# Kernel tuning notes

Hardware: AMD Instinct MI355X
Metric: run time of the kernel (lower is better)

## Reference

```python
import jax, jax.numpy as jnp
import numpy as np

B, T_PAST, FUTURE_N = 128, 1024, 512
IN_F, IP, H, OUT_F = 64, 128, 256, 64


def _init(key, shape, fan_in):
    return (jax.random.uniform(key, shape, jnp.float32) * 2.0 - 1.0) / np.sqrt(fan_in).astype(np.float32)


def setup_inputs() -> dict:
    key = jax.random.key(0)
    ks = jax.random.split(key, 16)
    return {
        "x": jax.random.normal(ks[0], (B, T_PAST, IN_F), jnp.float32),
        "future_n": FUTURE_N,
        # encoder: Linear(IN_F -> IP)
        "enc_W": _init(ks[1], (IP, IN_F), IN_F),
        "enc_b": _init(ks[2], (IP,), IN_F),
        # future encoder: Linear(H -> IP)
        "fut_W": _init(ks[3], (IP, H), H),
        "fut_b": _init(ks[4], (IP,), H),
        # decoder: Linear(H -> OUT_F)
        "dec_W": _init(ks[5], (OUT_F, H), H),
        "dec_b": _init(ks[6], (OUT_F,), H),
        # past LSTMCell(IP, H)
        "pW_ih": _init(ks[7], (4 * H, IP), H),
        "pW_hh": _init(ks[8], (4 * H, H), H),
        "pb_ih": _init(ks[9], (4 * H,), H),
        "pb_hh": _init(ks[10], (4 * H,), H),
        # future LSTMCell(IP, H)
        "fW_ih": _init(ks[11], (4 * H, IP), H),
        "fW_hh": _init(ks[12], (4 * H, H), H),
        "fb_ih": _init(ks[13], (4 * H,), H),
        "fb_hh": _init(ks[14], (4 * H,), H),
    }


def _lstm_cell(xt, h, c, W_ih, W_hh, b_ih, b_hh):
    # torch LSTMCell gate order: i, f, g, o
    gates = xt @ W_ih.T + h @ W_hh.T + (b_ih + b_hh)
    i, f, g, o = jnp.split(gates, 4, axis=-1)
    c_new = jax.nn.sigmoid(f) * c + jax.nn.sigmoid(i) * jnp.tanh(g)
    h_new = jax.nn.sigmoid(o) * jnp.tanh(c_new)
    return h_new, c_new


def reference(x, future_n, enc_W, enc_b, fut_W, fut_b, dec_W, dec_b,
              pW_ih, pW_hh, pb_ih, pb_hh, fW_ih, fW_hh, fb_ih, fb_hh):
    batch = x.shape[0]
    hidden = pW_hh.shape[1]
    h0 = jnp.zeros((batch, hidden), x.dtype)
    c0 = jnp.zeros((batch, hidden), x.dtype)

    encoded = x @ enc_W.T + enc_b  # [B, T, IP]

    def past_step(carry, xt):
        h, c = carry
        h, c = _lstm_cell(xt, h, c, pW_ih, pW_hh, pb_ih, pb_hh)
        return (h, c), h

    (h, c), hs_past = jax.lax.scan(past_step, (h0, c0), jnp.swapaxes(encoded, 0, 1))

    def fut_step(carry, _):
        h, c = carry
        inp = h @ fut_W.T + fut_b
        h, c = _lstm_cell(inp, h, c, fW_ih, fW_hh, fb_ih, fb_hh)
        return (h, c), h

    _, hs_fut = jax.lax.scan(fut_step, (h, c), None, length=future_n)

    hs = jnp.concatenate([hs_past, hs_fut], axis=0)  # [T+F, B, H]
    out = jnp.swapaxes(hs, 0, 1) @ dec_W.T + dec_b  # [B, T+F, OUT_F]
    return out
```

## Files before the change

### kernel.cpp

```cpp
#include <hip/hip_runtime.h>

#define B_    128
#define TPAST 1024
#define FN    512
#define TT    1536
#define INF   64
#define IPF   128
#define HD    256
#define NG    1024
#define OUTF  64

typedef _Float16 f16;
typedef _Float16 f16x8 __attribute__((ext_vector_type(8)));
typedef _Float16 f16x4 __attribute__((ext_vector_type(4)));
typedef float    f32x4 __attribute__((ext_vector_type(4)));

__device__ __forceinline__ float sigm_(float x) {
  return __builtin_amdgcn_rcpf(1.f + __expf(-x));
}
__device__ __forceinline__ float tanh_(float x) {
  return 1.f - 2.f * __builtin_amdgcn_rcpf(1.f + __expf(2.f * x));
}
__device__ __forceinline__ f16x8 oload16(const f16* p) {
  f16x8 v;
  asm volatile("global_load_dwordx4 %0, %1, off\n\ts_waitcnt vmcnt(0)"
               : "=v"(v) : "v"(p));
  return v;
}

extern "C" __global__ void eprep(
    const float* __restrict__ enc_W, const float* __restrict__ enc_b,
    const float* __restrict__ fut_W, const float* __restrict__ fut_b,
    const float* __restrict__ dec_W,
    const float* __restrict__ pW_ih, const float* __restrict__ pW_hh,
    const float* __restrict__ pb_ih, const float* __restrict__ pb_hh,
    const float* __restrict__ fW_ih, const float* __restrict__ fW_hh,
    const float* __restrict__ fb_ih, const float* __restrict__ fb_hh,
    f16* __restrict__ Wp_in, float* __restrict__ bp,
    f16* __restrict__ Wp16, f16* __restrict__ Wf16,
    float* __restrict__ bf, f16* __restrict__ dW16)
{
  int stride = gridDim.x * blockDim.x;
  int gid = blockIdx.x * blockDim.x + threadIdx.x;
  for (int i = gid; i < NG * HD; i += stride) {
    int n = i >> 8, j = i & 255;
    float s = fW_hh[i];
    for (int m = 0; m < IPF; ++m) s += fW_ih[n * IPF + m] * fut_W[m * HD + j];
    Wf16[i] = (f16)s;
    Wp16[i] = (f16)pW_hh[i];
  }
  for (int i = gid; i < NG * INF; i += stride) {
    int n = i >> 6, k = i & 63;
    float s = 0.f;
    for (int m = 0; m < IPF; ++m) s += pW_ih[n * IPF + m] * enc_W[m * INF + k];
    Wp_in[i] = (f16)s;
  }
  for (int i = gid; i < OUTF * HD; i += stride) dW16[i] = (f16)dec_W[i];
  for (int n = gid; n < NG; n += stride) {
    float s1 = pb_ih[n] + pb_hh[n], s2 = fb_ih[n] + fb_hh[n];
    for (int m = 0; m < IPF; ++m) {
      s1 += pW_ih[n * IPF + m] * enc_b[m];
      s2 += fW_ih[n * IPF + m] * fut_b[m];
    }
    bp[n] = s1; bf[n] = s2;
  }
}

extern "C" __global__ __launch_bounds__(64) void epgemm(
    const float* __restrict__ x, const f16* __restrict__ Wp_in,
    const float* __restrict__ bp, f16* __restrict__ P, int t0, int Tc)
{
  int wg = blockIdx.x;
  int tl = wg >> 3, bt = wg & 7;
  int t = t0 + tl;
  int l = (int)threadIdx.x, r = l & 15, g = l >> 4;
  const float* xb = x + ((size_t)(bt * 16 + r) * TPAST + t) * INF;
  f16x8 a[2];
#pragma unroll
  for (int kk = 0; kk < 2; ++kk) {
    const float* px = xb + kk * 32 + g * 8;
    f32x4 v0 = *(const f32x4*)px;
    f32x4 v1 = *(const f32x4*)(px + 4);
#pragma unroll
    for (int e = 0; e < 4; ++e) { a[kk][e] = (f16)v0[e]; a[kk][4 + e] = (f16)v1[e]; }
  }
  for (int nt = 0; nt < 64; ++nt) {
    int n = nt * 16 + r;
    f16x8 b0 = *(const f16x8*)(Wp_in + (size_t)n * INF + g * 8);
    f16x8 b1 = *(const f16x8*)(Wp_in + (size_t)n * INF + 32 + g * 8);
    f32x4 acc = {0.f, 0.f, 0.f, 0.f};
    acc = __builtin_amdgcn_mfma_f32_16x16x32_f16(a[0], b0, acc, 0, 0, 0);
    acc = __builtin_amdgcn_mfma_f32_16x16x32_f16(a[1], b1, acc, 0, 0, 0);
    float bias = bp[n];
    f16x4 hv;
#pragma unroll
    for (int e = 0; e < 4; ++e) hv[e] = (f16)(acc[e] + bias);
    int jh = (n >> 7) & 1;
    int nl = (n >> 8) * 128 + (n & 127);
    f16* Pt = P + (((size_t)(bt * 2 + jh) * Tc + tl) * 512 + nl) * 16;
    *(f16x4*)(Pt + 4 * g) = hv;
  }
}

extern "C" __global__ __launch_bounds__(256, 1)
void erecur(
    const f16* __restrict__ W, const f16* __restrict__ P, int pstep,
    const float* __restrict__ bias,
    f16* __restrict__ hs, f16* __restrict__ h_state, float* __restrict__ c_state,
    f16* __restrict__ Hx, unsigned int* __restrict__ flags,
    int Tc, int seq0, int init_state)
{
  __shared__ f16  Wl[512 * 96];
  __shared__ f16  hb[16 * HD];
  __shared__ float cb[128 * 20];
  __shared__ f16  bl[512];

  int tid = (int)threadIdx.x;
  int w = tid >> 6, l = tid & 63, r = l & 15, g = l >> 4;
  int wg = blockIdx.x;
  int bs = wg >> 1, jh = wg & 1;
  int b0 = bs * 16;

  for (int nl = tid; nl < 512; nl += 256) {
    int n_glob = (nl >> 7) * 256 + jh * 128 + (nl & 127);
#pragma unroll
    for (int c8 = 0; c8 < 12; ++c8) {
      f16x8 v = *(const f16x8*)(W + (size_t)n_glob * HD + 160 + c8 * 8);
      *(f16x8*)&Wl[(nl * 96 + c8 * 8) ^ ((nl & 7) << 3)] = v;
    }
  }
  if (bias) {
    for (int i = tid; i < 512; i += 256) {
      int n_glob = (i >> 7) * 256 + jh * 128 + (i & 127);
      bl[i] = (f16)bias[n_glob];
    }
  }
  f16x8 wf[4][2][5];
#pragma unroll
  for (int ga = 0; ga < 4; ++ga)
#pragma unroll
    for (int s = 0; s < 2; ++s) {
      int n_glob = ga * 256 + jh * 128 + w * 32 + s * 16 + r;
#pragma unroll
      for (int kt = 0; kt < 5; ++kt)
        wf[ga][s][kt] = oload16(W + (size_t)n_glob * HD + kt * 32 + g * 8);
    }
  if (init_state) {
    for (int i = tid; i < 16 * HD; i += 256) hb[i ^ (((i >> 8) & 7) << 3)] = (f16)0.f;
    for (int i = tid; i < 128 * 20; i += 256) cb[i] = 0.f;
  } else {
    for (int i = tid; i < 16 * HD; i += 256) {
      int b = i >> 8, j = i & 255;
      hb[i ^ ((b & 7) << 3)] = h_state[(size_t)(b0 + b) * HD + j];
    }
    for (int i = tid; i < 16 * 128; i += 256) {
      int b = i >> 7, j = i & 127;
      cb[j * 20 + b] = c_state[(size_t)(b0 + b) * HD + jh * 128 + j];
    }
  }
  __syncthreads();

  const f16* Pw = P ? (P + (size_t)wg * Tc * pstep) : nullptr;

  for (int tl = 0; tl < Tc; ++tl) {
    int seq = seq0 + tl;
    f16x4 pv[4][2];
    if (P) {
#pragma unroll
      for (int ga = 0; ga < 4; ++ga)
#pragma unroll
        for (int s = 0; s < 2; ++s) {
          int nl = ga * 128 + w * 32 + s * 16 + r;
          pv[ga][s] = *(const f16x4*)(Pw + nl * 16 + 4 * g);
        }
    }
    f32x4 acc[4][2];
#pragma unroll
    for (int ga = 0; ga < 4; ++ga)
#pragma unroll
      for (int s = 0; s < 2; ++s) acc[ga][s] = f32x4{0.f, 0.f, 0.f, 0.f};

#pragma unroll
    for (int kt = 0; kt < 5; ++kt) {
      f16x8 a = *(const f16x8*)&hb[(r * HD + kt * 32 + g * 8) ^ ((r & 7) << 3)];
#pragma unroll
      for (int ga = 0; ga < 4; ++ga)
#pragma unroll
        for (int s = 0; s < 2; ++s)
          acc[ga][s] = __builtin_amdgcn_mfma_f32_16x16x32_f16(a, wf[ga][s][kt], acc[ga][s], 0, 0, 0);
    }
#pragma unroll
    for (int kt = 5; kt < 8; ++kt) {
      f16x8 a = *(const f16x8*)&hb[(r * HD + kt * 32 + g * 8) ^ ((r & 7) << 3)];
#pragma unroll
      for (int ga = 0; ga < 4; ++ga)
#pragma unroll
        for (int s = 0; s < 2; ++s) {
          int nl = ga * 128 + w * 32 + s * 16 + r;
          f16x8 bw = *(const f16x8*)&Wl[(nl * 96 + (kt - 5) * 32 + g * 8) ^ ((nl & 7) << 3)];
          acc[ga][s] = __builtin_amdgcn_mfma_f32_16x16x32_f16(a, bw, acc[ga][s], 0, 0, 0);
        }
    }
    __syncthreads();

    f16* HxW = Hx + ((size_t)(seq & 1) * 16 + wg) * 2048;
#pragma unroll
    for (int s = 0; s < 2; ++s) {
      int j = w * 32 + s * 16 + r;
      int jg = jh * 128 + j;
      f32x4 cold = *(f32x4*)&cb[j * 20 + 4 * g];
      float gadd[4];
#pragma unroll
      for (int ga = 0; ga < 4; ++ga)
        gadd[ga] = P ? 0.f : (float)bl[ga * 128 + j];
      f32x4 cnew;
      union { unsigned long long u; f16 h4[4]; } pk;
#pragma unroll
      for (int e = 0; e < 4; ++e) {
        float xi = acc[0][s][e] + gadd[0];
        float xf = acc[1][s][e] + gadd[1];
        float xg = acc[2][s][e] + gadd[2];
        float xo = acc[3][s][e] + gadd[3];
        if (P) {
          xi += (float)pv[0][s][e]; xf += (float)pv[1][s][e];
          xg += (float)pv[2][s][e]; xo += (float)pv[3][s][e];
        }
        float ii = sigm_(xi), ff = sigm_(xf), oo = sigm_(xo), gg = tanh_(xg);
        float cn = ff * cold[e] + ii * gg;
        cnew[e] = cn;
        pk.h4[e] = (f16)(oo * tanh_(cn));
      }
      *(f32x4*)&cb[j * 20 + 4 * g] = cnew;
      __hip_atomic_store((unsigned long long*)(HxW + j * 16 + 4 * g), pk.u,
                         __ATOMIC_RELAXED, __HIP_MEMORY_SCOPE_AGENT);
#pragma unroll
      for (int e = 0; e < 4; ++e) {
        int b = 4 * g + e;
        hb[(b * HD + jg) ^ ((b & 7) << 3)] = pk.h4[e];
        hs[((size_t)tl * B_ + b0 + b) * HD + jg] = pk.h4[e];
      }
    }
    __syncthreads();

    if (tid == 0) {
      __hip_atomic_store(&flags[wg], (unsigned)(seq + 1),
                         __ATOMIC_RELEASE, __HIP_MEMORY_SCOPE_AGENT);
      while (__hip_atomic_load(&flags[wg ^ 1], __ATOMIC_ACQUIRE,
                               __HIP_MEMORY_SCOPE_AGENT) < (unsigned)(seq + 1)) {}
    }
    __syncthreads();

    const f16* HxR = Hx + ((size_t)(seq & 1) * 16 + (wg ^ 1)) * 2048;
#pragma unroll
    for (int u0 = 0; u0 < 2; ++u0) {
      int u = tid + u0 * 256;
      int j = u >> 2, q = u & 3;
      union { unsigned long long u64; f16 h4[4]; } pk;
      pk.u64 = __hip_atomic_load((const unsigned long long*)(HxR + j * 16 + q * 4),
                                 __ATOMIC_RELAXED, __HIP_MEMORY_SCOPE_AGENT);
      int jg = (jh ^ 1) * 128 + j;
#pragma unroll
      for (int e = 0; e < 4; ++e) {
        int b = q * 4 + e;
        hb[(b * HD + jg) ^ ((b & 7) << 3)] = pk.h4[e];
      }
    }
    __syncthreads();
    if (P) Pw += pstep;
  }
  for (int i = tid; i < 16 * 128; i += 256) {
    int b = i >> 7, j = i & 127;
    int jg = jh * 128 + j;
    h_state[(size_t)(b0 + b) * HD + jg] = hb[(b * HD + jg) ^ ((b & 7) << 3)];
    c_state[(size_t)(b0 + b) * HD + jg] = cb[j * 20 + b];
  }
}

extern "C" __global__ __launch_bounds__(64) void edec(
    const f16* __restrict__ hs, const f16* __restrict__ dW,
    const float* __restrict__ dec_b, float* __restrict__ out, int t0, int Tc)
{
  int wg = blockIdx.x;
  int tt = wg >> 7, b = wg & 127;
  int l = (int)threadIdx.x, r = l & 15, g = l >> 4;
  f16x8 wfr[4][8];
#pragma unroll
  for (int nt = 0; nt < 4; ++nt)
#pragma unroll
    for (int kt = 0; kt < 8; ++kt)
      wfr[nt][kt] = *(const f16x8*)(dW + (size_t)(nt * 16 + r) * HD + kt * 32 + g * 8);
  float bb[4];
#pragma unroll
  for (int nt = 0; nt < 4; ++nt) bb[nt] = dec_b[nt * 16 + r];
  f32x4 acc[2][4];
  const f32x4 zero4 = {0.f, 0.f, 0.f, 0.f};
#pragma unroll
  for (int mt = 0; mt < 2; ++mt)
#pragma unroll
    for (int nt = 0; nt < 4; ++nt) acc[mt][nt] = zero4;
#pragma unroll
  for (int mt = 0; mt < 2; ++mt)
#pragma unroll
    for (int kt = 0; kt < 8; ++kt) {
      f16x8 a = *(const f16x8*)(hs + ((size_t)(tt * 32 + mt * 16 + r) * B_ + b) * HD + kt * 32 + g * 8);
#pragma unroll
      for (int nt = 0; nt < 4; ++nt)
        acc[mt][nt] = __builtin_amdgcn_mfma_f32_16x16x32_f16(a, wfr[nt][kt], acc[mt][nt], 0, 0, 0);
    }
#pragma unroll
  for (int mt = 0; mt < 2; ++mt)
#pragma unroll
    for (int nt = 0; nt < 4; ++nt)
#pragma unroll
      for (int e = 0; e < 4; ++e) {
        int t = t0 + tt * 32 + mt * 16 + 4 * g + e;
        out[((size_t)b * TT + t) * OUTF + nt * 16 + r] = acc[mt][nt][e] + bb[nt];
      }
}

extern "C" void kernel_launch(void* const* d_in, const int* in_sizes, int n_in,
                              void* d_out, int out_size, void* d_ws, size_t ws_size,
                              hipStream_t stream)
{
  const float* x     = (const float*)d_in[0];
  const float* enc_W = (const float*)d_in[2];
  const float* enc_b = (const float*)d_in[3];
  const float* fut_W = (const float*)d_in[4];
  const float* fut_b = (const float*)d_in[5];
  const float* dec_W = (const float*)d_in[6];
  const float* dec_b = (const float*)d_in[7];
  const float* pW_ih = (const float*)d_in[8];
  const float* pW_hh = (const float*)d_in[9];
  const float* pb_ih = (const float*)d_in[10];
  const float* pb_hh = (const float*)d_in[11];
  const float* fW_ih = (const float*)d_in[12];
  const float* fW_hh = (const float*)d_in[13];
  const float* fb_ih = (const float*)d_in[14];
  const float* fb_hh = (const float*)d_in[15];
  (void)in_sizes; (void)n_in; (void)out_size;

  char* p = (char*)d_ws;
  auto alloc = [&](size_t bytes) { char* q = p; p += (bytes + 255) & ~(size_t)255; return q; };
  f16*   Wp_in = (f16*)  alloc((size_t)NG * INF * 2);
  float* bp    = (float*)alloc((size_t)NG * 4);
  f16*   Wp16  = (f16*)  alloc((size_t)NG * HD * 2);
  f16*   Wf16  = (f16*)  alloc((size_t)NG * HD * 2);
  float* bfb   = (float*)alloc((size_t)NG * 4);
  f16*   dW16  = (f16*)  alloc((size_t)OUTF * HD * 2);
  f16*   h_st  = (f16*)  alloc((size_t)B_ * HD * 2);
  float* c_st  = (float*)alloc((size_t)B_ * HD * 4);
  f16*   Hx    = (f16*)  alloc((size_t)2 * 16 * 2048 * 2);
  unsigned int* flags = (unsigned int*)alloc(64);
  size_t fixed = (size_t)(p - (char*)d_ws);

  auto need = [&](int rr) {
    size_t pp = (size_t)(rr < TPAST ? rr : TPAST) * NG * B_ * 2;
    size_t hh = (size_t)rr * B_ * HD * 2;
    return pp + hh + 4096;
  };
  size_t avail = ws_size > fixed ? ws_size - fixed : 0;
  int R = 128;
  if (avail >= need(1536)) R = 1536;
  else if (avail >= need(512)) R = 512;
  else if (avail >= need(256)) R = 256;

  f16* Pbuf = (f16*)alloc((size_t)(R < TPAST ? R : TPAST) * NG * B_ * 2);
  f16* HS   = (f16*)alloc((size_t)R * B_ * HD * 2);

  hipMemsetAsync(flags, 0, 64, stream);

  eprep<<<512, 256, 0, stream>>>(enc_W, enc_b, fut_W, fut_b, dec_W,
                                 pW_ih, pW_hh, pb_ih, pb_hh,
                                 fW_ih, fW_hh, fb_ih, fb_hh,
                                 Wp_in, bp, Wp16, Wf16, bfb, dW16);

  for (int t0 = 0; t0 < TPAST; t0 += R) {
    int Tc = (TPAST - t0) < R ? (TPAST - t0) : R;
    epgemm<<<Tc * 8, 64, 0, stream>>>(x, Wp_in, bp, Pbuf, t0, Tc);
    erecur<<<16, 256, 0, stream>>>(Wp16, Pbuf, 512 * 16, nullptr, HS, h_st, c_st,
                                   Hx, flags, Tc, t0, t0 == 0 ? 1 : 0);
    edec<<<(Tc / 32) * B_, 64, 0, stream>>>(HS, dW16, dec_b, (float*)d_out, t0, Tc);
  }
  for (int t0 = TPAST; t0 < TT; t0 += R) {
    int Tc = (TT - t0) < R ? (TT - t0) : R;
    erecur<<<16, 256, 0, stream>>>(Wf16, nullptr, 0, bfb, HS, h_st, c_st,
                                   Hx, flags, Tc, t0, 0);
    edec<<<(Tc / 32) * B_, 64, 0, stream>>>(HS, dW16, dec_b, (float*)d_out, t0, Tc);
  }
}
```

Baseline: 7.053 ms.

## Overlap peer hidden-state exchange with local-half GEMM using double-buffered LDS

The hidden-state buffer in LDS is now double-buffered. Each workgroup first multiplies the K-slice of h it produced itself, then waits for its partner's flag and pulls in the partner's half, then finishes the remaining K-slices. This replaces the blocking exchange and the extra barriers at the end of each step. Partner workgroups are remapped to wg and wg^8, which likely places them on the same XCD so flag and Hx traffic can stay in a shared L2. The global hs store is moved after the flag release so it no longer delays the partner. The cost is more LDS, a more intricate ordering argument, and spin-waiting with s_sleep.

```diff
diff --git a/kernel.cpp b/kernel.cpp
--- a/kernel.cpp
+++ b/kernel.cpp
@@ -14,6 +14,8 @@
 typedef _Float16 f16x8 __attribute__((ext_vector_type(8)));
 typedef _Float16 f16x4 __attribute__((ext_vector_type(4)));
 typedef float    f32x4 __attribute__((ext_vector_type(4)));
+
+template<int N> struct ic { static constexpr int value = N; };
 
 __device__ __forceinline__ float sigm_(float x) {
   return __builtin_amdgcn_rcpf(1.f + __expf(-x));
@@ -97,7 +99,7 @@
     for (int e = 0; e < 4; ++e) hv[e] = (f16)(acc[e] + bias);
     int jh = (n >> 7) & 1;
     int nl = (n >> 8) * 128 + (n & 127);
-    f16* Pt = P + (((size_t)(bt * 2 + jh) * Tc + tl) * 512 + nl) * 16;
+    f16* Pt = P + (((size_t)(jh * 8 + bt) * Tc + tl) * 512 + nl) * 16;
     *(f16x4*)(Pt + 4 * g) = hv;
   }
 }
@@ -111,15 +113,16 @@
     int Tc, int seq0, int init_state)
 {
   __shared__ f16  Wl[512 * 96];
-  __shared__ f16  hb[16 * HD];
+  __shared__ f16  hb[2][16 * HD];
   __shared__ float cb[128 * 20];
   __shared__ f16  bl[512];
 
   int tid = (int)threadIdx.x;
   int w = tid >> 6, l = tid & 63, r = l & 15, g = l >> 4;
   int wg = blockIdx.x;
-  int bs = wg >> 1, jh = wg & 1;
+  int bs = wg & 7, jh = wg >> 3;
   int b0 = bs * 16;
+  int pwg = wg ^ 8;
 
   for (int nl = tid; nl < 512; nl += 256) {
     int n_glob = (nl >> 7) * 256 + jh * 128 + (nl & 127);
@@ -145,13 +148,14 @@
       for (int kt = 0; kt < 5; ++kt)
         wf[ga][s][kt] = oload16(W + (size_t)n_glob * HD + kt * 32 + g * 8);
     }
+  int cur0 = seq0 & 1;
   if (init_state) {
-    for (int i = tid; i < 16 * HD; i += 256) hb[i ^ (((i >> 8) & 7) << 3)] = (f16)0.f;
+    for (int i = tid; i < 16 * HD; i += 256) hb[cur0][i ^ (((i >> 8) & 7) << 3)] = (f16)0.f;
     for (int i = tid; i < 128 * 20; i += 256) cb[i] = 0.f;
   } else {
     for (int i = tid; i < 16 * HD; i += 256) {
       int b = i >> 8, j = i & 255;
-      hb[i ^ ((b & 7) << 3)] = h_state[(size_t)(b0 + b) * HD + j];
+      hb[cur0][i ^ ((b & 7) << 3)] = h_state[(size_t)(b0 + b) * HD + j];
     }
     for (int i = tid; i < 16 * 128; i += 256) {
       int b = i >> 7, j = i & 127;
@@ -163,7 +167,9 @@
   const f16* Pw = P ? (P + (size_t)wg * Tc * pstep) : nullptr;
 
   for (int tl = 0; tl < Tc; ++tl) {
-    int seq = seq0 + tl;
+    int v = seq0 + tl;
+    const f16* hbc = hb[v & 1];
+
     f16x4 pv[4][2];
     if (P) {
 #pragma unroll
@@ -180,30 +186,56 @@
 #pragma unroll
       for (int s = 0; s < 2; ++s) acc[ga][s] = f32x4{0.f, 0.f, 0.f, 0.f};
 
-#pragma unroll
-    for (int kt = 0; kt < 5; ++kt) {
-      f16x8 a = *(const f16x8*)&hb[(r * HD + kt * 32 + g * 8) ^ ((r & 7) << 3)];
+    auto gemm_kt = [&](auto ktc) {
+      constexpr int KT = decltype(ktc)::value;
+      f16x8 a = *(const f16x8*)&hbc[(r * HD + KT * 32 + g * 8) ^ ((r & 7) << 3)];
 #pragma unroll
       for (int ga = 0; ga < 4; ++ga)
 #pragma unroll
-        for (int s = 0; s < 2; ++s)
-          acc[ga][s] = __builtin_amdgcn_mfma_f32_16x16x32_f16(a, wf[ga][s][kt], acc[ga][s], 0, 0, 0);
-    }
-#pragma unroll
-    for (int kt = 5; kt < 8; ++kt) {
-      f16x8 a = *(const f16x8*)&hb[(r * HD + kt * 32 + g * 8) ^ ((r & 7) << 3)];
-#pragma unroll
-      for (int ga = 0; ga < 4; ++ga)
-#pragma unroll
         for (int s = 0; s < 2; ++s) {
-          int nl = ga * 128 + w * 32 + s * 16 + r;
-          f16x8 bw = *(const f16x8*)&Wl[(nl * 96 + (kt - 5) * 32 + g * 8) ^ ((nl & 7) << 3)];
-          acc[ga][s] = __builtin_amdgcn_mfma_f32_16x16x32_f16(a, bw, acc[ga][s], 0, 0, 0);
+          if constexpr (KT < 5) {
+            acc[ga][s] = __builtin_amdgcn_mfma_f32_16x16x32_f16(a, wf[ga][s][KT], acc[ga][s], 0, 0, 0);
+          } else {
+            int nl = ga * 128 + w * 32 + s * 16 + r;
+            f16x8 bw = *(const f16x8*)&Wl[(nl * 96 + (KT - 5) * 32 + g * 8) ^ ((nl & 7) << 3)];
+            acc[ga][s] = __builtin_amdgcn_mfma_f32_16x16x32_f16(a, bw, acc[ga][s], 0, 0, 0);
+          }
         }
-    }
-    __syncthreads();
-
-    f16* HxW = Hx + ((size_t)(seq & 1) * 16 + wg) * 2048;
+    };
+
+    if (jh == 0) { gemm_kt(ic<0>{}); gemm_kt(ic<1>{}); gemm_kt(ic<2>{}); gemm_kt(ic<3>{}); }
+    else         { gemm_kt(ic<4>{}); gemm_kt(ic<5>{}); gemm_kt(ic<6>{}); gemm_kt(ic<7>{}); }
+
+    if (tl > 0) {
+      unsigned tgt = (unsigned)v;
+      while (__hip_atomic_load(&flags[pwg], __ATOMIC_ACQUIRE,
+                               __HIP_MEMORY_SCOPE_AGENT) < tgt)
+        __builtin_amdgcn_s_sleep(1);
+      const f16* HxR = Hx + ((size_t)(v & 1) * 16 + pwg) * 2048;
+      f16* hbw = hb[v & 1];
+#pragma unroll
+      for (int u0 = 0; u0 < 2; ++u0) {
+        int u = tid + u0 * 256;
+        int j = u >> 2, q = u & 3;
+        union { unsigned long long u64; f16 h4[4]; } pk;
+        pk.u64 = __hip_atomic_load((const unsigned long long*)(HxR + j * 16 + q * 4),
+                                   __ATOMIC_RELAXED, __HIP_MEMORY_SCOPE_AGENT);
+        int jg = (jh ^ 1) * 128 + j;
+#pragma unroll
+        for (int e = 0; e < 4; ++e) {
+          int b = q * 4 + e;
+          hbw[(b * HD + jg) ^ ((b & 7) << 3)] = pk.h4[e];
+        }
+      }
+      __syncthreads();
+    }
+
+    if (jh == 0) { gemm_kt(ic<4>{}); gemm_kt(ic<5>{}); gemm_kt(ic<6>{}); gemm_kt(ic<7>{}); }
+    else         { gemm_kt(ic<0>{}); gemm_kt(ic<1>{}); gemm_kt(ic<2>{}); gemm_kt(ic<3>{}); }
+
+    f16* hbn = hb[(v + 1) & 1];
+    f16* HxW = Hx + ((size_t)((v + 1) & 1) * 16 + wg) * 2048;
+    f16 hsave[2][4];
 #pragma unroll
     for (int s = 0; s < 2; ++s) {
       int j = w * 32 + s * 16 + r;
@@ -229,6 +261,7 @@
         float cn = ff * cold[e] + ii * gg;
         cnew[e] = cn;
         pk.h4[e] = (f16)(oo * tanh_(cn));
+        hsave[s][e] = pk.h4[e];
       }
       *(f32x4*)&cb[j * 20 + 4 * g] = cnew;
       __hip_atomic_store((unsigned long long*)(HxW + j * 16 + 4 * g), pk.u,
@@ -236,42 +269,29 @@
 #pragma unroll
       for (int e = 0; e < 4; ++e) {
         int b = 4 * g + e;
-        hb[(b * HD + jg) ^ ((b & 7) << 3)] = pk.h4[e];
-        hs[((size_t)tl * B_ + b0 + b) * HD + jg] = pk.h4[e];
+        hbn[(b * HD + jg) ^ ((b & 7) << 3)] = pk.h4[e];
       }
     }
     __syncthreads();
 
-    if (tid == 0) {
-      __hip_atomic_store(&flags[wg], (unsigned)(seq + 1),
+    if (tid == 0)
+      __hip_atomic_store(&flags[wg], (unsigned)(v + 1),
                          __ATOMIC_RELEASE, __HIP_MEMORY_SCOPE_AGENT);
-      while (__hip_atomic_load(&flags[wg ^ 1], __ATOMIC_ACQUIRE,
-                               __HIP_MEMORY_SCOPE_AGENT) < (unsigned)(seq + 1)) {}
-    }
-    __syncthreads();
-
-    const f16* HxR = Hx + ((size_t)(seq & 1) * 16 + (wg ^ 1)) * 2048;
-#pragma unroll
-    for (int u0 = 0; u0 < 2; ++u0) {
-      int u = tid + u0 * 256;
-      int j = u >> 2, q = u & 3;
-      union { unsigned long long u64; f16 h4[4]; } pk;
-      pk.u64 = __hip_atomic_load((const unsigned long long*)(HxR + j * 16 + q * 4),
-                                 __ATOMIC_RELAXED, __HIP_MEMORY_SCOPE_AGENT);
-      int jg = (jh ^ 1) * 128 + j;
-#pragma unroll
-      for (int e = 0; e < 4; ++e) {
-        int b = q * 4 + e;
-        hb[(b * HD + jg) ^ ((b & 7) << 3)] = pk.h4[e];
-      }
-    }
-    __syncthreads();
+
+#pragma unroll
+    for (int s = 0; s < 2; ++s) {
+      int jg = jh * 128 + w * 32 + s * 16 + r;
+#pragma unroll
+      for (int e = 0; e < 4; ++e)
+        hs[((size_t)tl * B_ + b0 + 4 * g + e) * HD + jg] = hsave[s][e];
+    }
     if (P) Pw += pstep;
   }
+  const f16* hbf = hb[(seq0 + Tc) & 1];
   for (int i = tid; i < 16 * 128; i += 256) {
     int b = i >> 7, j = i & 127;
     int jg = jh * 128 + j;
-    h_state[(size_t)(b0 + b) * HD + jg] = hb[(b * HD + jg) ^ ((b & 7) << 3)];
+    h_state[(size_t)(b0 + b) * HD + jg] = hbf[(b * HD + jg) ^ ((b & 7) << 3)];
     c_state[(size_t)(b0 + b) * HD + jg] = cb[j * 20 + b];
   }
 }
```

New measurement: 6.443 ms. -8.6%, faster.
